# Kernel optimization log

Hardware: AMD Instinct MI355X
Metric: run time of the kernel (lower is better)

Reference implementation:

```python
import jax, jax.numpy as jnp
import numpy as np
from jax import lax

D_MODEL = 2048
D_SSM = 4096          # expand * d_model
D_STATE = 128
NHEADS = 64
HEADDIM = 64          # D_SSM // NHEADS
NGROUPS = 1
D_CONV = 4
CHUNK = 64
D_IN_PROJ = 2 * D_SSM + 2 * NGROUPS * D_STATE + NHEADS   # 8512
CONV_DIM = D_SSM + 2 * NGROUPS * D_STATE                 # 4352
EPS = 1e-5


def setup_inputs() -> dict:
    key = jax.random.key(0)
    ks = jax.random.split(key, 10)
    B, L = 2, 4096
    u = jax.random.normal(ks[0], (B, L, D_MODEL), dtype=jnp.float32)
    W_in = jax.random.normal(ks[1], (D_IN_PROJ, D_MODEL), dtype=jnp.float32) * 0.02
    conv_w = jax.random.normal(ks[2], (CONV_DIM, D_CONV), dtype=jnp.float32) * 0.2
    conv_b = jax.random.normal(ks[3], (CONV_DIM,), dtype=jnp.float32) * 0.02
    # dt_bias ~ inverse-softplus of dt in [1e-3, 0.1]
    dt = jnp.exp(jax.random.uniform(ks[4], (NHEADS,), minval=np.log(1e-3), maxval=np.log(0.1)))
    dt_bias = dt + jnp.log(-jnp.expm1(-dt))
    # A ~ U(1, 16) -> A_log
    A_log = jnp.log(jax.random.uniform(ks[5], (NHEADS,), minval=1.0, maxval=16.0))
    D = jnp.ones((NHEADS,), dtype=jnp.float32)
    norm_weight = jnp.ones((D_SSM,), dtype=jnp.float32)
    W_out = jax.random.normal(ks[6], (D_MODEL, D_SSM), dtype=jnp.float32) * 0.02
    return {"u": u, "W_in": W_in, "conv_w": conv_w, "conv_b": conv_b,
            "dt_bias": dt_bias, "A_log": A_log, "D": D,
            "norm_weight": norm_weight, "W_out": W_out}


def _segsum(x):
    """x: [..., l] -> [..., l, l] with out[i,j] = sum_{k=j+1..i} x[k], -inf above diag."""
    l = x.shape[-1]
    cs = jnp.cumsum(x, axis=-1)
    seg = cs[..., :, None] - cs[..., None, :]
    mask = jnp.tril(jnp.ones((l, l), dtype=bool))
    return jnp.where(mask, seg, -jnp.inf)


def reference(u, W_in, conv_w, conv_b, dt_bias, A_log, D, norm_weight, W_out):
    b, L, _ = u.shape
    zxbcdt = jnp.einsum('bld,ed->ble', u, W_in)          # [b, L, 8512]
    z = zxbcdt[..., :D_SSM]                              # gate
    xBC = zxbcdt[..., D_SSM:D_SSM + CONV_DIM]
    dt = zxbcdt[..., -NHEADS:]                           # [b, L, h]

    # depthwise causal conv1d (kernel D_CONV) + SiLU
    xp = jnp.pad(xBC, ((0, 0), (D_CONV - 1, 0), (0, 0)))
    conv = conv_b
    for k in range(D_CONV):
        conv = conv + xp[:, k:k + L, :] * conv_w[:, k]
    xBC = jax.nn.silu(conv)

    x = xBC[..., :D_SSM].reshape(b, L, NHEADS, HEADDIM)
    Bm = xBC[..., D_SSM:D_SSM + D_STATE]                 # ngroups=1: [b, L, n]
    Cm = xBC[..., D_SSM + D_STATE:]

    dt = jax.nn.softplus(dt + dt_bias)                   # [b, L, h]
    A = -jnp.exp(A_log)                                  # [h]

    c = L // CHUNK
    xc = x.reshape(b, c, CHUNK, NHEADS, HEADDIM)
    dtc = dt.reshape(b, c, CHUNK, NHEADS)
    Bc = Bm.reshape(b, c, CHUNK, D_STATE)
    Cc = Cm.reshape(b, c, CHUNK, D_STATE)

    dA = dtc * A                                         # [b, c, l, h]
    A_cum = jnp.cumsum(dA, axis=2)

    # intra-chunk (diagonal) blocks
    Lmat = jnp.exp(_segsum(dA.transpose(0, 1, 3, 2)))    # [b, c, h, l, s]
    CB = jnp.einsum('bcln,bcsn->bcls', Cc, Bc)           # [b, c, l, s]
    Y_diag = jnp.einsum('bcls,bchls,bcsh,bcshp->bclhp', CB, Lmat, dtc, xc)

    # per-chunk final states
    decay_states = jnp.exp(A_cum[:, :, -1:, :] - A_cum)  # [b, c, l, h]
    states = jnp.einsum('bcln,bclh,bclhp->bchpn', Bc, decay_states * dtc, xc)

    # inter-chunk recurrence over chunks
    chunk_decay = jnp.exp(A_cum[:, :, -1, :])            # [b, c, h]

    def step(carry, inp):
        s, cd = inp                                      # s: [b,h,p,n], cd: [b,h]
        new = carry * cd[:, :, None, None] + s
        return new, carry                                # emit state BEFORE this chunk

    init = jnp.zeros((b, NHEADS, HEADDIM, D_STATE), dtype=u.dtype)
    _, prev = lax.scan(step, init, (states.transpose(1, 0, 2, 3, 4),
                                    chunk_decay.transpose(1, 0, 2)))
    prev = prev.transpose(1, 0, 2, 3, 4)                 # [b, c, h, p, n]

    Y_off = jnp.einsum('bcln,bchpn,bclh->bclhp', Cc, prev, jnp.exp(A_cum))

    y = (Y_diag + Y_off + xc * D[None, None, None, :, None]).reshape(b, L, D_SSM)

    # gated RMSNorm (norm_before_gate=False): rmsnorm(y * silu(z)) * weight
    yg = y * jax.nn.silu(z)
    var = jnp.mean(yg * yg, axis=-1, keepdims=True)
    y = yg * lax.rsqrt(var + EPS) * norm_weight

    return jnp.einsum('bld,ed->ble', y, W_out)
```

## Files before the change

### kernel.cpp

```cpp
#include <hip/hip_runtime.h>

typedef unsigned short u16;
typedef __attribute__((ext_vector_type(4))) float f4;
typedef __attribute__((ext_vector_type(8))) __bf16 bf16x8;
typedef __attribute__((ext_vector_type(4))) float f32x4;

#define D_MODEL 2048
#define D_SSM 4096
#define D_STATE 128
#define NHEADS 64
#define HEADDIM 64
#define CHUNK 64
#define LTOT 4096
#define NB 2
#define CONV_DIM 4352
#define XBC_LD 4480
#define LOG2E 1.4426950408889634f

__device__ inline float bf2f(unsigned v) { return __uint_as_float(v << 16); }
__device__ inline u16 f2bf(float f) {
    unsigned u = __float_as_uint(f);
    unsigned r = (u + 0x7fffu + ((u >> 16) & 1u)) >> 16;
    return (u16)r;
}
__device__ inline unsigned pack2(float a, float b) {
    return (unsigned)f2bf(a) | ((unsigned)f2bf(b) << 16);
}
__device__ inline float fexp2(float x) {
    float r;
    asm("v_exp_f32 %0, %1" : "=v"(r) : "v"(x));
    return r;
}
__device__ inline unsigned cvtpk(float lo, float hi) {
    unsigned r;
    asm("v_cvt_pk_bf16_f32 %0, %1, %2" : "=v"(r) : "v"(lo), "v"(hi));
    return r;
}
__device__ inline void gload_lds16(const void* g, void* l) {
    __builtin_amdgcn_global_load_lds((const __attribute__((address_space(1))) void*)g,
                                     (__attribute__((address_space(3))) void*)l, 16, 0, 0);
}

__global__ __launch_bounds__(256) void tobf16_kernel(const float* __restrict__ src,
                                                     u16* __restrict__ dst, int n4) {
    int i = blockIdx.x * 256 + threadIdx.x;
    if (i < n4) {
        f4 v = ((const f4*)src)[i];
        uint2 pk;
        pk.x = pack2(v[0], v[1]);
        pk.y = pack2(v[2], v[3]);
        ((uint2*)dst)[i] = pk;
    }
}

__global__ __launch_bounds__(256) void winpad_kernel(const float* __restrict__ src,
                                                     u16* __restrict__ dst) {
    int i = blockIdx.x * 256 + threadIdx.x;
    if (i >= (8704 * 2048 / 4)) return;
    int col4 = i & 511;
    int row = i >> 9;
    f4 v = {0.f, 0.f, 0.f, 0.f};
    if (row < 8512) v = ((const f4*)src)[row * 512 + col4];
    uint2 pk;
    pk.x = pack2(v[0], v[1]);
    pk.y = pack2(v[2], v[3]);
    ((uint2*)dst)[i] = pk;
}

template <int OUT_BF16>
__global__ __launch_bounds__(512, 2) void gemm256(const u16* __restrict__ A,
                                                  const u16* __restrict__ Bm,
                                                  void* __restrict__ Cp,
                                                  int K, int ldC, int Nreal) {
    __shared__ __align__(16) u16 lds[2][32768];

    int t = threadIdx.x;
    int w = t >> 6, lane = t & 63;
    int fm = lane & 15, fq = lane >> 4;
    int wm = w >> 2, wn = w & 3;

    int gx = gridDim.x;
    int nwg = gx * gridDim.y;
    int orig = blockIdx.y * gx + blockIdx.x;
    int wg = (orig & 7) * (nwg >> 3) + (orig >> 3);
    int blockN = (wg % gx) * 256;
    int blockM = (wg / gx) * 256;

    int srow = t >> 3;
    int scol = ((((t & 7) << 4) ^ ((srow & 7) << 4)) >> 1);
    const u16* Asrc = A + (size_t)(blockM + srow) * K + scol;
    const u16* Bsrc = Bm + (size_t)(blockN + srow) * K + scol;

    f32x4 acc[8][4] = {};

    int kso0 = (((fq * 16) ^ ((fm & 7) << 4)) >> 1);
    int kso1 = (((64 + fq * 16) ^ ((fm & 7) << 4)) >> 1);

    int nt = K >> 6;
#pragma unroll
    for (int h = 0; h < 2; ++h)
#pragma unroll
        for (int s = 0; s < 2; ++s) {
            gload_lds16(Asrc + (size_t)(h * 128 + s * 64) * K,
                        &lds[0][(h * 128 + s * 64) * 64 + t * 8]);
            gload_lds16(Bsrc + (size_t)(h * 128 + s * 64) * K,
                        &lds[0][16384 + (h * 128 + s * 64) * 64 + t * 8]);
        }

    int d = 0;
    for (int kt = 0; kt < nt; ++kt, d ^= 1) {
        if (kt + 1 < nt) {
            int e = d ^ 1;
            const u16* a1 = Asrc + (kt + 1) * 64;
            const u16* b1 = Bsrc + (kt + 1) * 64;
#pragma unroll
            for (int h = 0; h < 2; ++h)
#pragma unroll
                for (int s = 0; s < 2; ++s) {
                    gload_lds16(a1 + (size_t)(h * 128 + s * 64) * K,
                                &lds[e][(h * 128 + s * 64) * 64 + t * 8]);
                    gload_lds16(b1 + (size_t)(h * 128 + s * 64) * K,
                                &lds[e][16384 + (h * 128 + s * 64) * 64 + t * 8]);
                }
            asm volatile("s_waitcnt vmcnt(8)" ::: "memory");
        } else {
            asm volatile("s_waitcnt vmcnt(0)" ::: "memory");
        }
        __syncthreads();

        const u16* aP = &lds[d][(wm * 128 + fm) * 64];
        const u16* bP = &lds[d][16384 + (wn * 64 + fm) * 64];
#pragma unroll
        for (int ks = 0; ks < 2; ++ks) {
            int kso = ks ? kso1 : kso0;
            bf16x8 bfv[4];
#pragma unroll
            for (int nf = 0; nf < 4; ++nf) bfv[nf] = *(const bf16x8*)(bP + nf * 1024 + kso);
#pragma unroll
            for (int mh = 0; mh < 2; ++mh) {
                bf16x8 af[4];
#pragma unroll
                for (int i = 0; i < 4; ++i)
                    af[i] = *(const bf16x8*)(aP + (mh * 4 + i) * 1024 + kso);
                __builtin_amdgcn_s_setprio(1);
#pragma unroll
                for (int i = 0; i < 4; ++i)
#pragma unroll
                    for (int nf = 0; nf < 4; ++nf)
                        acc[mh * 4 + i][nf] = __builtin_amdgcn_mfma_f32_16x16x32_bf16(
                            af[i], bfv[nf], acc[mh * 4 + i][nf], 0, 0, 0);
                __builtin_amdgcn_s_setprio(0);
            }
        }
        __syncthreads();
    }

    int rb = blockM + wm * 128 + fq * 4;
    int cb = blockN + wn * 64 + fm;
    if (OUT_BF16) {
        u16* C = (u16*)Cp;
#pragma unroll
        for (int i = 0; i < 8; ++i)
#pragma unroll
            for (int nf = 0; nf < 4; ++nf) {
                int col = cb + nf * 16;
                if (col < Nreal) {
#pragma unroll
                    for (int r = 0; r < 4; ++r)
                        C[(size_t)(rb + i * 16 + r) * ldC + col] = f2bf(acc[i][nf][r]);
                }
            }
    } else {
        float* C = (float*)Cp;
#pragma unroll
        for (int i = 0; i < 8; ++i)
#pragma unroll
            for (int nf = 0; nf < 4; ++nf) {
                int col = cb + nf * 16;
                if (col < Nreal) {
#pragma unroll
                    for (int r = 0; r < 4; ++r)
                        C[(size_t)(rb + i * 16 + r) * ldC + col] = acc[i][nf][r];
                }
            }
    }
}

__global__ __launch_bounds__(256) void conv_kernel(const u16* __restrict__ xbcdt,
                                                   const float* __restrict__ conv_w,
                                                   const float* __restrict__ conv_b,
                                                   u16* __restrict__ convO) {
    int ch = blockIdx.x * 256 + threadIdx.x;
    int row = blockIdx.y;
    int l = row & (LTOT - 1);
    f4 w = *(const f4*)&conv_w[ch * 4];
    float acc = conv_b[ch];
#pragma unroll
    for (int k = 0; k < 4; ++k) {
        int ls = l - 3 + k;
        if (ls >= 0) acc += bf2f(xbcdt[(size_t)(row - 3 + k) * XBC_LD + ch]) * w[k];
    }
    convO[(size_t)row * CONV_DIM + ch] = f2bf(acc / (1.f + __expf(-acc)));
}

__global__ __launch_bounds__(256) void dt_kernel(const u16* __restrict__ xbcdt,
                                                 const float* __restrict__ dt_bias,
                                                 float* __restrict__ dtp) {
    int idx = blockIdx.x * 256 + threadIdx.x;
    if (idx >= NB * LTOT * NHEADS) return;
    int row = idx >> 6, h = idx & 63;
    float x = bf2f(xbcdt[(size_t)row * XBC_LD + CONV_DIM + h]) + dt_bias[h];
    dtp[idx] = (x > 15.f) ? x : log1pf(__expf(x));
}

__global__ __launch_bounds__(256) void cb_kernel(const u16* __restrict__ convO,
                                                 float* __restrict__ CBb) {
    __shared__ u16 Bt[128 * 68];
    __shared__ u16 Ct[128 * 68];
    int bc = blockIdx.x;
    int c = bc & 63, b = bc >> 6;
    int rowbase = b * LTOT + c * CHUNK;
    int t = threadIdx.x;
#pragma unroll
    for (int i = 0; i < 32; i++) {
        int idx = i * 256 + t;
        int s = idx >> 7, n = idx & 127;
        Bt[n * 68 + s] = convO[(size_t)(rowbase + s) * CONV_DIM + D_SSM + n];
        Ct[n * 68 + s] = convO[(size_t)(rowbase + s) * CONV_DIM + D_SSM + D_STATE + n];
    }
    __syncthreads();
    int sq = t & 15, lq = t >> 4;
    f4 acc[4] = {};
#pragma unroll 4
    for (int n = 0; n < 128; n++) {
        ushort4 bv = *(const ushort4*)&Bt[n * 68 + sq * 4];
        ushort4 cv = *(const ushort4*)&Ct[n * 68 + lq * 4];
        f4 bf;
        bf[0] = bf2f(bv.x); bf[1] = bf2f(bv.y); bf[2] = bf2f(bv.z); bf[3] = bf2f(bv.w);
        float c0 = bf2f(cv.x), c1 = bf2f(cv.y), c2 = bf2f(cv.z), c3 = bf2f(cv.w);
        acc[0] += c0 * bf; acc[1] += c1 * bf; acc[2] += c2 * bf; acc[3] += c3 * bf;
    }
    float* outb = CBb + (size_t)bc * 4096;
#pragma unroll
    for (int j = 0; j < 4; j++) *(f4*)&outb[(lq * 4 + j) * 64 + sq * 4] = acc[j];
}

__global__ __launch_bounds__(256, 2) void ssm_mfma(const u16* __restrict__ convO,
                                                   const float* __restrict__ dtp,
                                                   const float* __restrict__ CBb,
                                                   const float* __restrict__ A_log,
                                                   const float* __restrict__ Dvec,
                                                   u16* __restrict__ ybf) {
    __shared__ __align__(16) u16 xT[2][16 * 72];
    __shared__ __align__(16) u16 BT[2][128 * 64];
    __shared__ __align__(16) u16 Sd[2][16 * 136];
    __shared__ __align__(16) float scal[2][256];

    int t = threadIdx.x;
    int w = t >> 6, lane = t & 63;
    int z = blockIdx.x;
    int pg = z & 3, h = (z >> 2) & 63, b = z >> 8;
    int pbase = h * 64 + pg * 16;
    float Ah2 = -__expf(A_log[h]) * LOG2E;
    float Dh = Dvec[h];

    int fm = lane & 15;
    int fq = lane >> 4;
    int fk = fq * 8;
    int sl = t & 63;
    int sq = t >> 6;
    int lq = t & 15;
    int no = t >> 4;

    f32x4 sacc[2] = {};

    const float* CBbase = CBb + (size_t)(b * 64) * 4096;
    int yl = 16 * w + fm;
    int btc0 = (32 * w + fm) * 64;
    int fm7 = fm & 7;

    bf16x8 afr[4];
    f4 cbr[2][2];
    {
        int rowbase = b * LTOT;
        const u16* rowp = convO + (size_t)rowbase * CONV_DIM;
        const u16* Cg = rowp + (size_t)yl * CONV_DIM + D_SSM + D_STATE;
#pragma unroll
        for (int kk = 0; kk < 4; ++kk) afr[kk] = *(const bf16x8*)(Cg + kk * 32 + fk);
        const float* CBrow = CBbase + yl * 64;
#pragma unroll
        for (int kk = 0; kk < 2; ++kk) {
            cbr[kk][0] = *(const f4*)&CBrow[kk * 32 + fk];
            cbr[kk][1] = *(const f4*)&CBrow[kk * 32 + fk + 4];
        }
        if (t < 64) {
            float dtv = dtp[(size_t)(rowbase + t) * 64 + h];
            float v = dtv * Ah2;
#pragma unroll
            for (int off = 1; off < 64; off <<= 1) {
                float pv = __shfl_up(v, off, 64);
                if (t >= off) v += pv;
            }
            float alast = __shfl(v, 63, 64);
            scal[0][t] = dtv;
            scal[0][64 + t] = v;
            scal[0][128 + t] = dtv * fexp2(alast - v);
            scal[0][192 + t] = fexp2(v);
        }
        ushort4 xv = *(const ushort4*)(rowp + (size_t)sl * CONV_DIM + pbase + sq * 4);
        xT[0][(sq * 4 + 0) * 72 + sl] = xv.x;
        xT[0][(sq * 4 + 1) * 72 + sl] = xv.y;
        xT[0][(sq * 4 + 2) * 72 + sl] = xv.z;
        xT[0][(sq * 4 + 3) * 72 + sl] = xv.w;
        {
            const u16* bp = rowp + D_SSM + no * 8;
            union { uint4 v; unsigned ww[4]; } q[4];
#pragma unroll
            for (int r = 0; r < 4; ++r) q[r].v = *(const uint4*)(bp + (size_t)(4 * lq + r) * CONV_DIM);
            int base = no * 512 + (lq & 1) * 4;
            int lqh = lq >> 1;
#pragma unroll
            for (int j = 0; j < 8; ++j) {
                unsigned sel = (j & 1) ? 0x07060302u : 0x05040100u;
                uint2 pk;
                pk.x = __builtin_amdgcn_perm(q[1].ww[j >> 1], q[0].ww[j >> 1], sel);
                pk.y = __builtin_amdgcn_perm(q[3].ww[j >> 1], q[2].ww[j >> 1], sel);
                *(uint2*)&BT[0][base + j * 64 + ((lqh ^ j) << 3)] = pk;
            }
        }
#pragma unroll
        for (int nt = 0; nt < 2; ++nt)
#pragma unroll
            for (int r = 0; r < 4; ++r)
                Sd[0][(fq * 4 + r) * 136 + 32 * w + 16 * nt + fm] = 0;
        __syncthreads();
    }

    f4 ydef = {0.f, 0.f, 0.f, 0.f};
    int cur = 0;
    for (int c = 0; c < 64; ++c, cur ^= 1) {
        int rowbase = b * LTOT + c * CHUNK;
        const u16* rowp = convO + (size_t)rowbase * CONV_DIM;

        if (c > 0) {
            unsigned y01 = cvtpk(ydef[0], ydef[1]);
            unsigned y23 = cvtpk(ydef[2], ydef[3]);
            u16* yp = ybf + (size_t)(rowbase - CHUNK + 16 * w + fq * 4) * D_SSM + pbase + fm;
            yp[0] = (u16)y01;
            yp[D_SSM] = (u16)(y01 >> 16);
            yp[2 * D_SSM] = (u16)y23;
            yp[3 * D_SSM] = (u16)(y23 >> 16);
        }

        bf16x8 afr_n[4] = {};
        f4 cbr_n[2][2] = {};
        uint4 bv0 = {}, bv1 = {}, bv2 = {}, bv3 = {};
        ushort4 xv = {0, 0, 0, 0};
        float dtv = 0.f;
        if (c < 63) {
            const u16* rowp1 = rowp + (size_t)CHUNK * CONV_DIM;
            const u16* Cg = rowp1 + (size_t)yl * CONV_DIM + D_SSM + D_STATE;
#pragma unroll
            for (int kk = 0; kk < 4; ++kk) afr_n[kk] = *(const bf16x8*)(Cg + kk * 32 + fk);
            const float* CBrow = CBbase + (size_t)(c + 1) * 4096 + yl * 64;
#pragma unroll
            for (int kk = 0; kk < 2; ++kk) {
                cbr_n[kk][0] = *(const f4*)&CBrow[kk * 32 + fk];
                cbr_n[kk][1] = *(const f4*)&CBrow[kk * 32 + fk + 4];
            }
            const u16* bp = rowp1 + D_SSM + no * 8;
            bv0 = *(const uint4*)(bp + (size_t)(4 * lq + 0) * CONV_DIM);
            bv1 = *(const uint4*)(bp + (size_t)(4 * lq + 1) * CONV_DIM);
            bv2 = *(const uint4*)(bp + (size_t)(4 * lq + 2) * CONV_DIM);
            bv3 = *(const uint4*)(bp + (size_t)(4 * lq + 3) * CONV_DIM);
            xv = *(const ushort4*)(rowp1 + (size_t)sl * CONV_DIM + pbase + sq * 4);
            if (t < 64) dtv = dtp[(size_t)(rowbase + CHUNK + t) * 64 + h];
        }

        const float* sc = scal[cur];
        const u16* xTc = xT[cur];
        const u16* BTc = BT[cur];
        const u16* Sdc = Sd[cur];

        union { uint4 v; u16 us[8]; bf16x8 bv; } xx0, xx1;
        xx0.v = *(const uint4*)&xTc[fm * 72 + fk];
        xx1.v = *(const uint4*)&xTc[fm * 72 + 32 + fk];
        ushort4 xe = *(const ushort4*)&xTc[fm * 72 + 16 * w + fq * 4];
        f4 els4 = *(const f4*)&sc[192 + 16 * w + fq * 4];
        float acl = sc[64 + yl];
        float cd = sc[192 + 63];
        f4 ac00 = *(const f4*)&sc[64 + fk], ac01 = *(const f4*)&sc[64 + fk + 4];
        f4 ac10 = *(const f4*)&sc[96 + fk], ac11 = *(const f4*)&sc[96 + fk + 4];
        f4 dt00 = *(const f4*)&sc[fk], dt01 = *(const f4*)&sc[fk + 4];
        f4 dt10 = *(const f4*)&sc[32 + fk], dt11 = *(const f4*)&sc[32 + fk + 4];
        f4 w00 = *(const f4*)&sc[128 + fk], w01 = *(const f4*)&sc[128 + fk + 4];
        f4 w10 = *(const f4*)&sc[160 + fk], w11 = *(const f4*)&sc[160 + fk + 4];
        bf16x8 sdf0 = *(const bf16x8*)&Sdc[fm * 136 + fk];
        bf16x8 sdf1 = *(const bf16x8*)&Sdc[fm * 136 + 32 + fk];
        bf16x8 sdf2 = *(const bf16x8*)&Sdc[fm * 136 + 64 + fk];
        bf16x8 sdf3 = *(const bf16x8*)&Sdc[fm * 136 + 96 + fk];
        int pb0 = (fq ^ fm7) << 3;
        int pb1 = ((4 + fq) ^ fm7) << 3;
        bf16x8 btf00 = *(const bf16x8*)&BTc[btc0 + pb0];
        bf16x8 btf01 = *(const bf16x8*)&BTc[btc0 + 1024 + pb0];
        bf16x8 btf10 = *(const bf16x8*)&BTc[btc0 + pb1];
        bf16x8 btf11 = *(const bf16x8*)&BTc[btc0 + 1024 + pb1];

        f32x4 ydia = {0.f, 0.f, 0.f, 0.f};
        {
            union { unsigned u[4]; bf16x8 v; } gu;
            float g[8];
#pragma unroll
            for (int j = 0; j < 4; ++j) {
                int s = fk + j;
                g[j] = (s <= yl) ? cbr[0][0][j] * fexp2(acl - ac00[j]) * dt00[j] : 0.f;
            }
#pragma unroll
            for (int j = 0; j < 4; ++j) {
                int s = fk + 4 + j;
                g[4 + j] = (s <= yl) ? cbr[0][1][j] * fexp2(acl - ac01[j]) * dt01[j] : 0.f;
            }
            gu.u[0] = cvtpk(g[0], g[1]);
            gu.u[1] = cvtpk(g[2], g[3]);
            gu.u[2] = cvtpk(g[4], g[5]);
            gu.u[3] = cvtpk(g[6], g[7]);
            ydia = __builtin_amdgcn_mfma_f32_16x16x32_bf16(gu.v, xx0.bv, ydia, 0, 0, 0);
#pragma unroll
            for (int j = 0; j < 4; ++j) {
                int s = 32 + fk + j;
                g[j] = (s <= yl) ? cbr[1][0][j] * fexp2(acl - ac10[j]) * dt10[j] : 0.f;
            }
#pragma unroll
            for (int j = 0; j < 4; ++j) {
                int s = 32 + fk + 4 + j;
                g[4 + j] = (s <= yl) ? cbr[1][1][j] * fexp2(acl - ac11[j]) * dt11[j] : 0.f;
            }
            gu.u[0] = cvtpk(g[0], g[1]);
            gu.u[1] = cvtpk(g[2], g[3]);
            gu.u[2] = cvtpk(g[4], g[5]);
            gu.u[3] = cvtpk(g[6], g[7]);
            ydia = __builtin_amdgcn_mfma_f32_16x16x32_bf16(gu.v, xx1.bv, ydia, 0, 0, 0);
        }

        sacc[0] *= cd;
        sacc[1] *= cd;
        {
            union { unsigned u[4]; bf16x8 v; } au;
            float xf[8];
#pragma unroll
            for (int j = 0; j < 8; ++j) xf[j] = bf2f(xx0.us[j]);
            au.u[0] = cvtpk(xf[0] * w00[0], xf[1] * w00[1]);
            au.u[1] = cvtpk(xf[2] * w00[2], xf[3] * w00[3]);
            au.u[2] = cvtpk(xf[4] * w01[0], xf[5] * w01[1]);
            au.u[3] = cvtpk(xf[6] * w01[2], xf[7] * w01[3]);
            sacc[0] = __builtin_amdgcn_mfma_f32_16x16x32_bf16(au.v, btf00, sacc[0], 0, 0, 0);
            sacc[1] = __builtin_amdgcn_mfma_f32_16x16x32_bf16(au.v, btf01, sacc[1], 0, 0, 0);
#pragma unroll
            for (int j = 0; j < 8; ++j) xf[j] = bf2f(xx1.us[j]);
            au.u[0] = cvtpk(xf[0] * w10[0], xf[1] * w10[1]);
            au.u[1] = cvtpk(xf[2] * w10[2], xf[3] * w10[3]);
            au.u[2] = cvtpk(xf[4] * w11[0], xf[5] * w11[1]);
            au.u[3] = cvtpk(xf[6] * w11[2], xf[7] * w11[3]);
            sacc[0] = __builtin_amdgcn_mfma_f32_16x16x32_bf16(au.v, btf10, sacc[0], 0, 0, 0);
            sacc[1] = __builtin_amdgcn_mfma_f32_16x16x32_bf16(au.v, btf11, sacc[1], 0, 0, 0);
        }

        f32x4 yoff = {0.f, 0.f, 0.f, 0.f};
        yoff = __builtin_amdgcn_mfma_f32_16x16x32_bf16(afr[0], sdf0, yoff, 0, 0, 0);
        yoff = __builtin_amdgcn_mfma_f32_16x16x32_bf16(afr[1], sdf1, yoff, 0, 0, 0);
        yoff = __builtin_amdgcn_mfma_f32_16x16x32_bf16(afr[2], sdf2, yoff, 0, 0, 0);
        yoff = __builtin_amdgcn_mfma_f32_16x16x32_bf16(afr[3], sdf3, yoff, 0, 0, 0);

        {
            float xf0 = bf2f(xe.x), xf1 = bf2f(xe.y), xf2 = bf2f(xe.z), xf3 = bf2f(xe.w);
            ydef[0] = yoff[0] * els4[0] + ydia[0] + Dh * xf0;
            ydef[1] = yoff[1] * els4[1] + ydia[1] + Dh * xf1;
            ydef[2] = yoff[2] * els4[2] + ydia[2] + Dh * xf2;
            ydef[3] = yoff[3] * els4[3] + ydia[3] + Dh * xf3;
        }

        if (c < 63) {
            int nxt = cur ^ 1;
            if (t < 64) {
                float v = dtv * Ah2;
#pragma unroll
                for (int off = 1; off < 64; off <<= 1) {
                    float pv = __shfl_up(v, off, 64);
                    if (t >= off) v += pv;
                }
                float alast = __shfl(v, 63, 64);
                scal[nxt][t] = dtv;
                scal[nxt][64 + t] = v;
                scal[nxt][128 + t] = dtv * fexp2(alast - v);
                scal[nxt][192 + t] = fexp2(v);
            }
            xT[nxt][(sq * 4 + 0) * 72 + sl] = xv.x;
            xT[nxt][(sq * 4 + 1) * 72 + sl] = xv.y;
            xT[nxt][(sq * 4 + 2) * 72 + sl] = xv.z;
            xT[nxt][(sq * 4 + 3) * 72 + sl] = xv.w;
            {
                union { uint4 v; unsigned ww[4]; } q0, q1, q2, q3;
                q0.v = bv0; q1.v = bv1; q2.v = bv2; q3.v = bv3;
                int base = no * 512 + (lq & 1) * 4;
                int lqh = lq >> 1;
#pragma unroll
                for (int j = 0; j < 8; ++j) {
                    unsigned sel = (j & 1) ? 0x07060302u : 0x05040100u;
                    uint2 pk;
                    pk.x = __builtin_amdgcn_perm(q1.ww[j >> 1], q0.ww[j >> 1], sel);
                    pk.y = __builtin_amdgcn_perm(q3.ww[j >> 1], q2.ww[j >> 1], sel);
                    *(uint2*)&BT[nxt][base + j * 64 + ((lqh ^ j) << 3)] = pk;
                }
            }
#pragma unroll
            for (int nt = 0; nt < 2; ++nt) {
                unsigned p01 = cvtpk(sacc[nt][0], sacc[nt][1]);
                unsigned p23 = cvtpk(sacc[nt][2], sacc[nt][3]);
                int colb = 32 * w + 16 * nt + fm;
                Sd[nxt][(fq * 4 + 0) * 136 + colb] = (u16)p01;
                Sd[nxt][(fq * 4 + 1) * 136 + colb] = (u16)(p01 >> 16);
                Sd[nxt][(fq * 4 + 2) * 136 + colb] = (u16)p23;
                Sd[nxt][(fq * 4 + 3) * 136 + colb] = (u16)(p23 >> 16);
            }
        }
        __syncthreads();

#pragma unroll
        for (int kk = 0; kk < 4; ++kk) afr[kk] = afr_n[kk];
#pragma unroll
        for (int kk = 0; kk < 2; ++kk) {
            cbr[kk][0] = cbr_n[kk][0];
            cbr[kk][1] = cbr_n[kk][1];
        }
    }

    {
        unsigned y01 = cvtpk(ydef[0], ydef[1]);
        unsigned y23 = cvtpk(ydef[2], ydef[3]);
        u16* yp = ybf + (size_t)(b * LTOT + 63 * CHUNK + 16 * w + fq * 4) * D_SSM + pbase + fm;
        yp[0] = (u16)y01;
        yp[D_SSM] = (u16)(y01 >> 16);
        yp[2 * D_SSM] = (u16)y23;
        yp[3 * D_SSM] = (u16)(y23 >> 16);
    }
}

__global__ __launch_bounds__(256) void gate_norm(const u16* __restrict__ zbf,
                                                 const float* __restrict__ normw,
                                                 u16* __restrict__ ybf) {
    int row = blockIdx.x, t = threadIdx.x;
    const uint2* y2 = (const uint2*)(ybf + (size_t)row * D_SSM);
    const uint2* z2 = (const uint2*)(zbf + (size_t)row * D_SSM);
    f4 yg[4];
    float ss = 0.f;
#pragma unroll
    for (int i = 0; i < 4; ++i) {
        int idx = i * 256 + t;
        uint2 yv = y2[idx], zv = z2[idx];
        float ya[4] = {bf2f(yv.x & 0xffffu), bf2f(yv.x >> 16), bf2f(yv.y & 0xffffu), bf2f(yv.y >> 16)};
        float za[4] = {bf2f(zv.x & 0xffffu), bf2f(zv.x >> 16), bf2f(zv.y & 0xffffu), bf2f(zv.y >> 16)};
        f4 g;
#pragma unroll
        for (int k = 0; k < 4; ++k) {
            float sz = za[k] / (1.f + __expf(-za[k]));
            g[k] = ya[k] * sz;
            ss += g[k] * g[k];
        }
        yg[i] = g;
    }
#pragma unroll
    for (int off = 32; off; off >>= 1) ss += __shfl_down(ss, off, 64);
    __shared__ float red[4];
    if ((t & 63) == 0) red[t >> 6] = ss;
    __syncthreads();
    float tot = red[0] + red[1] + red[2] + red[3];
    float scale = rsqrtf(tot / (float)D_SSM + 1e-5f);
    const f4* nw4 = (const f4*)normw;
    uint2* out = (uint2*)(ybf + (size_t)row * D_SSM);
#pragma unroll
    for (int i = 0; i < 4; ++i) {
        int idx = i * 256 + t;
        f4 v = yg[i] * scale * nw4[idx];
        uint2 pk;
        pk.x = pack2(v[0], v[1]);
        pk.y = pack2(v[2], v[3]);
        out[idx] = pk;
    }
}

extern "C" void kernel_launch(void* const* d_in, const int* in_sizes, int n_in,
                              void* d_out, int out_size, void* d_ws, size_t ws_size,
                              hipStream_t stream) {
    const float* u = (const float*)d_in[0];
    const float* W_in = (const float*)d_in[1];
    const float* conv_w = (const float*)d_in[2];
    const float* conv_b = (const float*)d_in[3];
    const float* dt_bias = (const float*)d_in[4];
    const float* A_log = (const float*)d_in[5];
    const float* Dv = (const float*)d_in[6];
    const float* normw = (const float*)d_in[7];
    const float* W_out = (const float*)d_in[8];
    float* out = (float*)d_out;
    char* ws = (char*)d_ws;

    u16* z_bf = (u16*)(ws + 0ULL);
    u16* xbcdt = (u16*)(ws + 67108864ULL);
    u16* y_bf = xbcdt;
    u16* convO = (u16*)(ws + 140509184ULL);
    u16* u_bf = convO;
    u16* win_bf = (u16*)(ws + 174063616ULL);
    u16* wout_bf = convO;
    float* dtp = (float*)(ws + 211812352ULL);
    float* CBb = (float*)(ws + 213909504ULL);

    tobf16_kernel<<<16384, 256, 0, stream>>>(u, u_bf, 4194304);
    winpad_kernel<<<17408, 256, 0, stream>>>(W_in, win_bf);
    gemm256<1><<<dim3(16, 32), 512, 0, stream>>>(u_bf, win_bf, z_bf, 2048, 4096, 4096);
    gemm256<1><<<dim3(18, 32), 512, 0, stream>>>(u_bf, win_bf + (size_t)4096 * 2048, xbcdt, 2048, XBC_LD, 4480);
    conv_kernel<<<dim3(17, 8192), 256, 0, stream>>>(xbcdt, conv_w, conv_b, convO);
    dt_kernel<<<2048, 256, 0, stream>>>(xbcdt, dt_bias, dtp);
    cb_kernel<<<128, 256, 0, stream>>>(convO, CBb);
    ssm_mfma<<<512, 256, 0, stream>>>(convO, dtp, CBb, A_log, Dv, y_bf);
    tobf16_kernel<<<8192, 256, 0, stream>>>(W_out, wout_bf, 2097152);
    gate_norm<<<8192, 256, 0, stream>>>(z_bf, normw, y_bf);
    gemm256<0><<<dim3(8, 32), 512, 0, stream>>>(y_bf, wout_bf, out, 4096, 2048, 2048);
}
```

Baseline: 1.034 ms.

## Restructure 256x256 GEMM main loop into four quadrant sub-phases with staggered half-tile loads

Rewrites the bf16 GEMM mainloop so each K-tile is processed as four 128x128 quadrants. Each wave computes a 64x32 piece of every quadrant, so the per-wave output is split into strided 16-row and 16-column fragments rather than one contiguous 128x64 block. Global-to-LDS loads for the next tiles are issued in half-tile pieces between quadrant phases, with finer vmcnt waits and raw s_barrier in place of __syncthreads, so memory traffic overlaps more evenly with MFMA work. Fragment reuse is reduced (A fragments are reloaded per half) and barrier count rises, and launch bounds drop to one block per CU, trading occupancy for register headroom.

```diff
diff --git a/kernel.cpp b/kernel.cpp
--- a/kernel.cpp
+++ b/kernel.cpp
@@ -39,6 +39,9 @@
 __device__ inline void gload_lds16(const void* g, void* l) {
     __builtin_amdgcn_global_load_lds((const __attribute__((address_space(1))) void*)g,
                                      (__attribute__((address_space(3))) void*)l, 16, 0, 0);
+}
+__device__ inline f32x4 mfma16(bf16x8 a, bf16x8 b, f32x4 c) {
+    return __builtin_amdgcn_mfma_f32_16x16x32_bf16(a, b, c, 0, 0, 0);
 }
 
 __global__ __launch_bounds__(256) void tobf16_kernel(const float* __restrict__ src,
@@ -68,7 +71,7 @@
 }
 
 template <int OUT_BF16>
-__global__ __launch_bounds__(512, 2) void gemm256(const u16* __restrict__ A,
+__global__ __launch_bounds__(512, 1) void gemm256(const u16* __restrict__ A,
                                                   const u16* __restrict__ Bm,
                                                   void* __restrict__ Cp,
                                                   int K, int ldC, int Nreal) {
@@ -87,102 +90,150 @@
     int blockM = (wg / gx) * 256;
 
     int srow = t >> 3;
-    int scol = ((((t & 7) << 4) ^ ((srow & 7) << 4)) >> 1);
+    int scol = (((t & 7) ^ (srow & 7)) << 3);
     const u16* Asrc = A + (size_t)(blockM + srow) * K + scol;
     const u16* Bsrc = Bm + (size_t)(blockN + srow) * K + scol;
 
+#define STAGE(buf, isB, half, tile)                                              \
+    do {                                                                         \
+        const u16* _s = ((isB) ? Bsrc : Asrc) + (size_t)(tile) * 64 +            \
+                        (size_t)((half) * 128) * K;                              \
+        u16* _d = &lds[buf][(isB) * 16384 + (half) * 8192 + t * 8];              \
+        gload_lds16(_s, _d);                                                     \
+        gload_lds16(_s + (size_t)64 * K, _d + 4096);                             \
+    } while (0)
+
+    int nt = K >> 6;
+    STAGE(0, 0, 0, 0); STAGE(0, 1, 0, 0);
+    STAGE(0, 0, 1, 0); STAGE(0, 1, 1, 0);
+    STAGE(1, 0, 0, 1); STAGE(1, 1, 0, 1);
+
     f32x4 acc[8][4] = {};
-
-    int kso0 = (((fq * 16) ^ ((fm & 7) << 4)) >> 1);
-    int kso1 = (((64 + fq * 16) ^ ((fm & 7) << 4)) >> 1);
-
-    int nt = K >> 6;
-#pragma unroll
-    for (int h = 0; h < 2; ++h)
-#pragma unroll
-        for (int s = 0; s < 2; ++s) {
-            gload_lds16(Asrc + (size_t)(h * 128 + s * 64) * K,
-                        &lds[0][(h * 128 + s * 64) * 64 + t * 8]);
-            gload_lds16(Bsrc + (size_t)(h * 128 + s * 64) * K,
-                        &lds[0][16384 + (h * 128 + s * 64) * 64 + t * 8]);
-        }
-
-    int d = 0;
-    for (int kt = 0; kt < nt; ++kt, d ^= 1) {
-        if (kt + 1 < nt) {
-            int e = d ^ 1;
-            const u16* a1 = Asrc + (kt + 1) * 64;
-            const u16* b1 = Bsrc + (kt + 1) * 64;
-#pragma unroll
-            for (int h = 0; h < 2; ++h)
-#pragma unroll
-                for (int s = 0; s < 2; ++s) {
-                    gload_lds16(a1 + (size_t)(h * 128 + s * 64) * K,
-                                &lds[e][(h * 128 + s * 64) * 64 + t * 8]);
-                    gload_lds16(b1 + (size_t)(h * 128 + s * 64) * K,
-                                &lds[e][16384 + (h * 128 + s * 64) * 64 + t * 8]);
+    int lro = fm * 64;
+    int ko0 = ((fq ^ (fm & 7)) << 3);
+    int ko1 = (((4 + fq) ^ (fm & 7)) << 3);
+
+    asm volatile("s_waitcnt vmcnt(8)" ::: "memory");
+    __builtin_amdgcn_s_barrier();
+
+    for (int kt = 0; kt < nt; ++kt) {
+        int d = kt & 1, e = d ^ 1;
+        const u16* aH0 = &lds[d][wm * 4096 + lro];
+        const u16* aH1 = aH0 + 8192;
+        const u16* bH0 = &lds[d][16384 + wn * 2048 + lro];
+        const u16* bH1 = bH0 + 8192;
+        bf16x8 af[4][2], bfr[2][2];
+
+#pragma unroll
+        for (int i = 0; i < 4; ++i) {
+            af[i][0] = *(const bf16x8*)(aH0 + i * 1024 + ko0);
+            af[i][1] = *(const bf16x8*)(aH0 + i * 1024 + ko1);
+        }
+#pragma unroll
+        for (int j = 0; j < 2; ++j) {
+            bfr[j][0] = *(const bf16x8*)(bH0 + j * 1024 + ko0);
+            bfr[j][1] = *(const bf16x8*)(bH0 + j * 1024 + ko1);
+        }
+        if (kt + 1 < nt) STAGE(e, 0, 1, kt + 1);
+        __builtin_amdgcn_s_barrier();
+        __builtin_amdgcn_s_setprio(1);
+#pragma unroll
+        for (int i = 0; i < 4; ++i)
+#pragma unroll
+            for (int j = 0; j < 2; ++j) {
+                acc[i][j] = mfma16(af[i][0], bfr[j][0], acc[i][j]);
+                acc[i][j] = mfma16(af[i][1], bfr[j][1], acc[i][j]);
+            }
+        __builtin_amdgcn_s_setprio(0);
+        if (kt == nt - 1) asm volatile("s_waitcnt vmcnt(0)" ::: "memory");
+        else              asm volatile("s_waitcnt vmcnt(6)" ::: "memory");
+        __builtin_amdgcn_s_barrier();
+
+#pragma unroll
+        for (int j = 0; j < 2; ++j) {
+            bfr[j][0] = *(const bf16x8*)(bH1 + j * 1024 + ko0);
+            bfr[j][1] = *(const bf16x8*)(bH1 + j * 1024 + ko1);
+        }
+        if (kt + 1 < nt) STAGE(e, 1, 1, kt + 1);
+        __builtin_amdgcn_s_barrier();
+        __builtin_amdgcn_s_setprio(1);
+#pragma unroll
+        for (int i = 0; i < 4; ++i)
+#pragma unroll
+            for (int j = 0; j < 2; ++j) {
+                acc[i][2 + j] = mfma16(af[i][0], bfr[j][0], acc[i][2 + j]);
+                acc[i][2 + j] = mfma16(af[i][1], bfr[j][1], acc[i][2 + j]);
+            }
+        __builtin_amdgcn_s_setprio(0);
+        __builtin_amdgcn_s_barrier();
+
+#pragma unroll
+        for (int i = 0; i < 4; ++i) {
+            af[i][0] = *(const bf16x8*)(aH1 + i * 1024 + ko0);
+            af[i][1] = *(const bf16x8*)(aH1 + i * 1024 + ko1);
+        }
+#pragma unroll
+        for (int j = 0; j < 2; ++j) {
+            bfr[j][0] = *(const bf16x8*)(bH0 + j * 1024 + ko0);
+            bfr[j][1] = *(const bf16x8*)(bH0 + j * 1024 + ko1);
+        }
+        if (kt + 2 < nt) STAGE(d, 0, 0, kt + 2);
+        __builtin_amdgcn_s_barrier();
+        __builtin_amdgcn_s_setprio(1);
+#pragma unroll
+        for (int i = 0; i < 4; ++i)
+#pragma unroll
+            for (int j = 0; j < 2; ++j) {
+                acc[4 + i][j] = mfma16(af[i][0], bfr[j][0], acc[4 + i][j]);
+                acc[4 + i][j] = mfma16(af[i][1], bfr[j][1], acc[4 + i][j]);
+            }
+        __builtin_amdgcn_s_setprio(0);
+        __builtin_amdgcn_s_barrier();
+
+#pragma unroll
+        for (int j = 0; j < 2; ++j) {
+            bfr[j][0] = *(const bf16x8*)(bH1 + j * 1024 + ko0);
+            bfr[j][1] = *(const bf16x8*)(bH1 + j * 1024 + ko1);
+        }
+        if (kt + 2 < nt) STAGE(d, 1, 0, kt + 2);
+        __builtin_amdgcn_s_barrier();
+        __builtin_amdgcn_s_setprio(1);
+#pragma unroll
+        for (int i = 0; i < 4; ++i)
+#pragma unroll
+            for (int j = 0; j < 2; ++j) {
+                acc[4 + i][2 + j] = mfma16(af[i][0], bfr[j][0], acc[4 + i][2 + j]);
+                acc[4 + i][2 + j] = mfma16(af[i][1], bfr[j][1], acc[4 + i][2 + j]);
+            }
+        __builtin_amdgcn_s_setprio(0);
+        if (kt == nt - 2)      asm volatile("s_waitcnt vmcnt(4)" ::: "memory");
+        else if (kt < nt - 2)  asm volatile("s_waitcnt vmcnt(8)" ::: "memory");
+        __builtin_amdgcn_s_barrier();
+    }
+#undef STAGE
+
+#pragma unroll
+    for (int i = 0; i < 8; ++i) {
+        int rbase = (i < 4) ? (wm * 64 + i * 16) : (128 + wm * 64 + (i - 4) * 16);
+        int row = blockM + rbase + fq * 4;
+#pragma unroll
+        for (int j = 0; j < 4; ++j) {
+            int cbase = (j < 2) ? (wn * 32 + j * 16) : (128 + wn * 32 + (j - 2) * 16);
+            int col = blockN + cbase + fm;
+            if (col < Nreal) {
+                if (OUT_BF16) {
+                    u16* C = (u16*)Cp;
+#pragma unroll
+                    for (int r = 0; r < 4; ++r)
+                        C[(size_t)(row + r) * ldC + col] = f2bf(acc[i][j][r]);
+                } else {
+                    float* C = (float*)Cp;
+#pragma unroll
+                    for (int r = 0; r < 4; ++r)
+                        C[(size_t)(row + r) * ldC + col] = acc[i][j][r];
                 }
-            asm volatile("s_waitcnt vmcnt(8)" ::: "memory");
-        } else {
-            asm volatile("s_waitcnt vmcnt(0)" ::: "memory");
-        }
-        __syncthreads();
-
-        const u16* aP = &lds[d][(wm * 128 + fm) * 64];
-        const u16* bP = &lds[d][16384 + (wn * 64 + fm) * 64];
-#pragma unroll
-        for (int ks = 0; ks < 2; ++ks) {
-            int kso = ks ? kso1 : kso0;
-            bf16x8 bfv[4];
-#pragma unroll
-            for (int nf = 0; nf < 4; ++nf) bfv[nf] = *(const bf16x8*)(bP + nf * 1024 + kso);
-#pragma unroll
-            for (int mh = 0; mh < 2; ++mh) {
-                bf16x8 af[4];
-#pragma unroll
-                for (int i = 0; i < 4; ++i)
-                    af[i] = *(const bf16x8*)(aP + (mh * 4 + i) * 1024 + kso);
-                __builtin_amdgcn_s_setprio(1);
-#pragma unroll
-                for (int i = 0; i < 4; ++i)
-#pragma unroll
-                    for (int nf = 0; nf < 4; ++nf)
-                        acc[mh * 4 + i][nf] = __builtin_amdgcn_mfma_f32_16x16x32_bf16(
-                            af[i], bfv[nf], acc[mh * 4 + i][nf], 0, 0, 0);
-                __builtin_amdgcn_s_setprio(0);
-            }
-        }
-        __syncthreads();
-    }
-
-    int rb = blockM + wm * 128 + fq * 4;
-    int cb = blockN + wn * 64 + fm;
-    if (OUT_BF16) {
-        u16* C = (u16*)Cp;
-#pragma unroll
-        for (int i = 0; i < 8; ++i)
-#pragma unroll
-            for (int nf = 0; nf < 4; ++nf) {
-                int col = cb + nf * 16;
-                if (col < Nreal) {
-#pragma unroll
-                    for (int r = 0; r < 4; ++r)
-                        C[(size_t)(rb + i * 16 + r) * ldC + col] = f2bf(acc[i][nf][r]);
-                }
-            }
-    } else {
-        float* C = (float*)Cp;
-#pragma unroll
-        for (int i = 0; i < 8; ++i)
-#pragma unroll
-            for (int nf = 0; nf < 4; ++nf) {
-                int col = cb + nf * 16;
-                if (col < Nreal) {
-#pragma unroll
-                    for (int r = 0; r < 4; ++r)
-                        C[(size_t)(rb + i * 16 + r) * ldC + col] = acc[i][nf][r];
-                }
-            }
+            }
+        }
     }
 }
 
```

Result: faster. 972.6 us (-5.9%).
